# Kernel tuning notes

Measured on AMD Instinct MI355X. Metric: run time of the kernel, lower is better.

## Reference

```python
import jax, jax.numpy as jnp
import numpy as np

LOCAL_SIZE = 128
LN_EPS = 1e-5


def _ln(x):
    # F.layer_norm over last axis, no affine params
    mu = jnp.mean(x, axis=-1, keepdims=True)
    var = jnp.var(x, axis=-1, keepdims=True)
    return (x - mu) / jnp.sqrt(var + LN_EPS)


def _rel_shift(x):
    # x: [b, n, qlen, klen] -> Transformer-XL relative shift
    b, n, q, k = x.shape
    xp = jnp.pad(x, ((0, 0), (0, 0), (0, 0), (1, 0)))
    xp = xp.reshape(b, n, k + 1, q)
    return xp[:, :, 1:, :].reshape(b, n, q, k)


def setup_inputs() -> dict:
    key = jax.random.key(0)
    ks = jax.random.split(key, 12)
    bsz, d_model, qlen, mlen = 16, 1024, 256, 256
    n_head, d_head, d_inner = 16, 64, 4096
    klen = qlen + mlen
    s = 0.02  # param init scale
    return {
        "z1ss": jax.random.normal(ks[0], (bsz, d_model, qlen), jnp.float32),
        "uss": jax.random.normal(ks[1], (bsz, 3 * n_head * d_head, klen), jnp.float32) * 0.1,
        "mems": jax.random.normal(ks[2], (bsz, d_model, mlen), jnp.float32),
        "pos_emb": jax.random.normal(ks[3], (d_model, klen), jnp.float32),
        "Wqkv": jax.random.normal(ks[4], (3 * n_head * d_head, d_model), jnp.float32) * s,
        "Wr": jax.random.normal(ks[5], (n_head * d_head, d_model), jnp.float32) * s,
        "Wo": jax.random.normal(ks[6], (d_model, n_head * d_head), jnp.float32) * s,
        "bo": jnp.zeros((d_model,), jnp.float32),
        "r_w_bias": jax.random.uniform(ks[7], (n_head, d_head), jnp.float32, -0.05, 0.05),
        "r_r_bias": jax.random.uniform(ks[8], (n_head, d_head), jnp.float32, -0.05, 0.05),
        "W1": jax.random.normal(ks[9], (d_inner, d_model), jnp.float32) * s,
        "b1": jnp.zeros((d_inner,), jnp.float32),
        "W2": jax.random.normal(ks[10], (d_model, d_inner), jnp.float32) * s,
        "b2": jnp.zeros((d_model,), jnp.float32),
    }


def reference(z1ss, uss, mems, pos_emb, Wqkv, Wr, Wo, bo, r_w_bias, r_r_bias, W1, b1, W2, b2):
    bsz, d_model, qlen = z1ss.shape
    mlen = mems.shape[-1]
    n_head, d_head = r_w_bias.shape
    scale = 1.0 / (d_head ** 0.5)

    # ---- self-attention with relative positions ----
    cat = jnp.concatenate([mems, z1ss], axis=-1)            # [b, d, klen]
    klen = cat.shape[-1]
    w_heads = jnp.einsum('od,bdk->bok', Wqkv, cat) + uss     # [b, 3*n*dh, klen]
    r_head_k = (Wr @ pos_emb).reshape(n_head, d_head, -1)    # [n, dh, rlen]

    q, k, v = jnp.split(w_heads, 3, axis=1)
    q = q[:, :, -qlen:].reshape(bsz, n_head, d_head, qlen)   # [b, n, dh, q]
    k = k.reshape(bsz, n_head, d_head, klen)
    v = v.reshape(bsz, n_head, d_head, klen)

    AC = jnp.einsum('bndi,bndj->bnij', q + r_w_bias[:, :, None], k)
    BD = jnp.einsum('bndi,ndj->bnij', q + r_r_bias[:, :, None], r_head_k)
    BD = _rel_shift(BD)
    attn_score = (AC + BD) * scale                            # [b, n, q, klen]

    # causal + local-window mask
    i = jnp.arange(qlen)[:, None]
    j = jnp.arange(klen)[None, :]
    mask = (j > i + mlen) | (j <= i + mlen - LOCAL_SIZE)      # [q, klen]
    attn_score = jnp.where(mask[None, None], -1e30, attn_score)

    attn_prob = jax.nn.softmax(attn_score, axis=-1)
    attn_vec = jnp.einsum('bnij,bndj->bndi', attn_prob, v)    # [b, n, dh, q]
    attn_vec = attn_vec.reshape(bsz, n_head * d_head, qlen)
    attn_out = jnp.einsum('od,bdq->boq', Wo, attn_vec) + bo[None, :, None]

    # post-LN residual (pre_lnorm=False), work in [b, q, d]
    h = _ln((attn_out + z1ss).transpose(0, 2, 1))             # [b, q, d]

    # ---- position-wise FF ----
    ff = jax.nn.relu(jnp.einsum('bqd,id->bqi', h, W1) + b1)
    ff = jnp.einsum('bqi,di->bqd', ff, W2) + b2
    out = _ln(ff + h)                                          # [b, q, d]
    return out.transpose(0, 2, 1)                              # [b, d, q]
```

## Files before the change

### kernel.cpp

```cpp
#include <hip/hip_runtime.h>
#include <hip/hip_bf16.h>
#include <math.h>

#define BSZ    16
#define DMODEL 1024
#define QLEN   256
#define MLEN   256
#define KLEN   512
#define NHEAD  16
#define DHEAD  64
#define DINNER 4096

typedef __bf16 bf16;
typedef bf16 bf16x8 __attribute__((ext_vector_type(8)));
typedef float f32x4 __attribute__((ext_vector_type(4)));

#define GLOBAL_AS __attribute__((address_space(1)))
#define LDS_AS    __attribute__((address_space(3)))

__global__ __launch_bounds__(256) void prep_flat_k(
    const float* __restrict__ w0, const float* __restrict__ w1,
    const float* __restrict__ w2, const float* __restrict__ w3,
    const float* __restrict__ w4, const float* __restrict__ uss,
    bf16* __restrict__ o0, bf16* __restrict__ o1, bf16* __restrict__ o2,
    bf16* __restrict__ o3, bf16* __restrict__ o4, bf16* __restrict__ oV)
{
    long long i = (long long)blockIdx.x * 256 + threadIdx.x;
    const float* src; bf16* dst; long long soff, doff;
    if      (i <  786432) { src = w0; dst = o0; soff = doff = i; }
    else if (i < 1048576) { src = w1; dst = o1; soff = doff = i -  786432; }
    else if (i < 1310720) { src = w2; dst = o2; soff = doff = i - 1048576; }
    else if (i < 2359296) { src = w3; dst = o3; soff = doff = i - 1310720; }
    else if (i < 3407872) { src = w4; dst = o4; soff = doff = i - 2359296; }
    else {
        long long u = i - 3407872, b = u >> 17, r = u & 131071;
        src = uss; dst = oV; soff = b * 393216 + 262144 + r; doff = u;
    }
    float4 v = ((const float4*)src)[soff];
    bf16 b0 = (bf16)v.x, b1 = (bf16)v.y, b2 = (bf16)v.z, b3 = (bf16)v.w;
    union { ushort u[4]; uint2 d; } p;
    p.u[0] = *(ushort*)&b0; p.u[1] = *(ushort*)&b1;
    p.u[2] = *(ushort*)&b2; p.u[3] = *(ushort*)&b3;
    ((uint2*)dst)[doff] = p.d;
}

__global__ __launch_bounds__(256) void prep_tr_k(
    const float* __restrict__ mems, const float* __restrict__ z1ss,
    const float* __restrict__ pos_emb, const float* __restrict__ uss,
    bf16* __restrict__ catT, bf16* __restrict__ posT,
    bf16* __restrict__ ussQ, bf16* __restrict__ ussK)
{
    __shared__ float tile[32][33];
    int blk = blockIdx.x;
    const float* src; bf16* dst; long long soff, dof; int ld, ldo, tr, tc;
    if (blk < 8192) {
        int bh = blk >> 8, t = blk & 255;
        int b = bh >> 1, half = bh & 1;
        tr = t >> 3; tc = t & 7;
        src = half ? z1ss : mems; soff = (long long)b * 1024 * 256; ld = 256;
        dst = catT; dof = ((long long)b * 512 + half * 256) * 1024; ldo = 1024;
    } else if (blk < 8704) {
        int u = blk - 8192; tr = u >> 4; tc = u & 15;
        src = pos_emb; soff = 0; ld = 512;
        dst = posT; dof = 0; ldo = 1024;
    } else if (blk < 12800) {
        int u = blk - 8704; int b = u >> 8, t = u & 255;
        tr = t >> 3; tc = t & 7;
        src = uss; soff = (long long)b * 3072 * 512 + 256; ld = 512;
        dst = ussQ; dof = (long long)b * 256 * 1024; ldo = 1024;
    } else {
        int u = blk - 12800; int b = u >> 9, t = u & 511;
        tr = t >> 4; tc = t & 15;
        src = uss; soff = ((long long)b * 3072 + 1024) * 512; ld = 512;
        dst = ussK; dof = (long long)b * 512 * 1024; ldo = 1024;
    }
    int tx = threadIdx.x & 31, ty = threadIdx.x >> 5;
    const float* ip = src + soff;
#pragma unroll
    for (int yy = ty; yy < 32; yy += 8)
        tile[yy][tx] = ip[(long long)(tr * 32 + yy) * ld + tc * 32 + tx];
    __syncthreads();
#pragma unroll
    for (int yy = ty; yy < 32; yy += 8)
        dst[dof + (long long)(tc * 32 + yy) * ldo + tr * 32 + tx] = (bf16)tile[tx][yy];
}

__global__ __launch_bounds__(256) void gemm_bf16(
    const bf16* __restrict__ A, long long aBatch,
    const bf16* __restrict__ B, long long bBatch,
    int M, int N, int K, int kChunk,
    const float* __restrict__ bias,
    const bf16* __restrict__ Eb, long long ebBatch,
    int relu,
    float* __restrict__ outF, long long ofBatch,
    bf16* __restrict__ outB, long long obBatch,
    int omode, bf16* __restrict__ outB2,
    const bf16* __restrict__ EbQ, const bf16* __restrict__ EbK,
    const bf16* __restrict__ A2, const bf16* __restrict__ B2,
    bf16* __restrict__ O2)
{
    int t = threadIdx.x;
    int w = t >> 6, lane = t & 63;
    int m0 = blockIdx.y * 128, n0 = blockIdx.x * 128;
    int bz = blockIdx.z;
    bool rhk = (omode == 1) && (bz == 16);

    if (omode == 1 && !rhk && m0 < 256 && n0 < 1024) return;
    if (rhk && n0 >= 1024) return;

    __shared__ bf16 lA[128 * 32];
    __shared__ bf16 lB[128 * 32];

    const bf16* Ap; const bf16* Bp;
    float* oF = outF;
    bf16*  oB = outB;
    const bf16* Ebp = Eb;
    int Keff = K;
    if (rhk) {
        Ap = A2; Bp = B2;
    } else if (kChunk > 0) {
        Ap = A + (long long)bz * kChunk;
        Bp = B + (long long)bz * kChunk;
        if (outF) oF = outF + (long long)bz * ofBatch;
        Keff = kChunk;
    } else {
        Ap = A + (long long)bz * aBatch;
        Bp = B + (long long)bz * bBatch;
        if (Eb)   Ebp = Eb + (long long)bz * ebBatch;
        if (outF) oF = outF + (long long)bz * ofBatch;
        if (outB && omode == 0) oB = outB + (long long)bz * obBatch;
    }

    int q = lane >> 4, r16 = lane & 15;
    int wm = w >> 1, wn = w & 1;

    f32x4 acc[4][4];
#pragma unroll
    for (int i = 0; i < 4; ++i)
#pragma unroll
        for (int j = 0; j < 4; ++j)
            acc[i][j] = (f32x4){0.f, 0.f, 0.f, 0.f};

    int srow = (lane >> 2);
    int scol = (lane & 3) * 8;

    for (int k0 = 0; k0 < Keff; k0 += 32) {
        __syncthreads();
#pragma unroll
        for (int issue = 0; issue < 2; ++issue) {
            int c = issue * 4 + w;
            int row = c * 16 + srow;
            __builtin_amdgcn_global_load_lds(
                (const GLOBAL_AS void*)(Ap + (long long)(m0 + row) * K + k0 + scol),
                (LDS_AS void*)(lA + c * 512 + lane * 8), 16, 0, 0);
            __builtin_amdgcn_global_load_lds(
                (const GLOBAL_AS void*)(Bp + (long long)(n0 + row) * K + k0 + scol),
                (LDS_AS void*)(lB + c * 512 + lane * 8), 16, 0, 0);
        }
        __syncthreads();

        bf16x8 af[4], bfr[4];
#pragma unroll
        for (int i = 0; i < 4; ++i)
            af[i] = *(const bf16x8*)&lA[(wm * 64 + i * 16 + r16) * 32 + q * 8];
#pragma unroll
        for (int j = 0; j < 4; ++j)
            bfr[j] = *(const bf16x8*)&lB[(wn * 64 + j * 16 + r16) * 32 + q * 8];
#pragma unroll
        for (int i = 0; i < 4; ++i)
#pragma unroll
            for (int j = 0; j < 4; ++j)
                acc[i][j] = __builtin_amdgcn_mfma_f32_16x16x32_bf16(
                    af[i], bfr[j], acc[i][j], 0, 0, 0);
    }

#pragma unroll
    for (int i = 0; i < 4; ++i) {
#pragma unroll
        for (int r = 0; r < 4; ++r) {
            int m = m0 + wm * 64 + i * 16 + q * 4 + r;
#pragma unroll
            for (int j = 0; j < 4; ++j) {
                int n = n0 + wn * 64 + j * 16 + r16;
                float v = acc[i][j][r];
                if (bias) v += bias[n];
                if (relu) v = fmaxf(v, 0.f);
                if (rhk) {
                    O2[(long long)m * 1024 + n] = (bf16)v;
                } else if (omode == 1) {
                    if (n < 1024) {
                        if (m >= 256) {
                            long long idx = ((long long)(bz * 256 + m - 256) << 10) + n;
                            outB[idx] = (bf16)(v + (float)EbQ[idx]);
                        }
                    } else {
                        long long idx = ((long long)(bz * 512 + m) << 10) + (n - 1024);
                        outB2[idx] = (bf16)(v + (float)EbK[idx]);
                    }
                } else {
                    if (Eb) v += (float)Ebp[(long long)m * N + n];
                    if (oF) oF[(long long)m * N + n] = v;
                    if (oB) oB[(long long)m * N + n] = (bf16)v;
                }
            }
        }
    }
}

__global__ __launch_bounds__(256) void attn_mfma_k(
    const bf16* __restrict__ qT,
    const bf16* __restrict__ kT,
    const bf16* __restrict__ vB,
    const bf16* __restrict__ rhkT,
    const float* __restrict__ rwb,
    const float* __restrict__ rrb,
    bf16* __restrict__ avT)
{
    __shared__ float sBD[64][132];

    int t = threadIdx.x;
    int w = t >> 6, lane = t & 63;
    int lo = lane & 15, hi = lane >> 4;
    int i0 = blockIdx.x * 64;
    int n  = blockIdx.y;
    int b  = blockIdx.z;

    const bf16* qp = qT + ((long long)(b * 256 + i0 + 16 * w + lo)) * 1024 + n * 64;
    bf16x8 qw[2], qr[2];
#pragma unroll
    for (int ks = 0; ks < 2; ++ks) {
        bf16x8 qv = *(const bf16x8*)(qp + ks * 32 + hi * 8);
        const float* wb = rwb + n * 64 + ks * 32 + hi * 8;
        const float* rb = rrb + n * 64 + ks * 32 + hi * 8;
#pragma unroll
        for (int e = 0; e < 8; ++e) {
            float qf = (float)qv[e];
            qw[ks][e] = (bf16)(qf + wb[e]);
            qr[ks][e] = (bf16)(qf + rb[e]);
        }
    }

    const bf16* rp = rhkT + (long long)384 * 1024 + n * 64;
#pragma unroll
    for (int tj = 0; tj < 8; ++tj) {
        const bf16* bp = rp + (long long)(16 * tj + lo) * 1024;
        f32x4 a = (f32x4){0.f, 0.f, 0.f, 0.f};
        a = __builtin_amdgcn_mfma_f32_16x16x32_bf16(qr[0], *(const bf16x8*)(bp + hi * 8), a, 0, 0, 0);
        a = __builtin_amdgcn_mfma_f32_16x16x32_bf16(qr[1], *(const bf16x8*)(bp + 32 + hi * 8), a, 0, 0, 0);
#pragma unroll
        for (int r = 0; r < 4; ++r)
            sBD[16 * w + hi * 4 + r][16 * tj + lo] = a[r];
    }
    __syncthreads();

    f32x4 ac[12];
    const bf16* kp = kT + ((long long)b * 512 + i0 + 129) * 1024 + n * 64;
#pragma unroll
    for (int tj = 0; tj < 12; ++tj) {
        const bf16* bp = kp + (long long)(16 * tj + lo) * 1024;
        f32x4 a = (f32x4){0.f, 0.f, 0.f, 0.f};
        a = __builtin_amdgcn_mfma_f32_16x16x32_bf16(qw[0], *(const bf16x8*)(bp + hi * 8), a, 0, 0, 0);
        a = __builtin_amdgcn_mfma_f32_16x16x32_bf16(qw[1], *(const bf16x8*)(bp + 32 + hi * 8), a, 0, 0, 0);
        ac[tj] = a;
    }

    float p[12][4], rowmax[4], rowsum[4];
#pragma unroll
    for (int r = 0; r < 4; ++r) rowmax[r] = -1e30f;
#pragma unroll
    for (int tj = 0; tj < 12; ++tj) {
#pragma unroll
        for (int r = 0; r < 4; ++r) {
            int m = 16 * w + hi * 4 + r;
            int jj = 16 * tj + lo;
            int tt = jj - m;
            float v = (tt >= 0 && tt < 128) ? (ac[tj][r] + sBD[m][tt]) * 0.125f
                                            : -1e30f;
            p[tj][r] = v;
            rowmax[r] = fmaxf(rowmax[r], v);
        }
    }
#pragma unroll
    for (int r = 0; r < 4; ++r) {
        float mx = rowmax[r];
#pragma unroll
        for (int msk = 1; msk < 16; msk <<= 1)
            mx = fmaxf(mx, __shfl_xor(mx, msk, 64));
        rowmax[r] = mx;
        rowsum[r] = 0.f;
    }
#pragma unroll
    for (int tj = 0; tj < 12; ++tj) {
#pragma unroll
        for (int r = 0; r < 4; ++r) {
            float e = exp2f((p[tj][r] - rowmax[r]) * 1.44269504f);
            p[tj][r] = e;
            rowsum[r] += e;
        }
    }
#pragma unroll
    for (int r = 0; r < 4; ++r) {
        float s = rowsum[r];
#pragma unroll
        for (int msk = 1; msk < 16; msk <<= 1)
            s += __shfl_xor(s, msk, 64);
        rowsum[r] = 1.f / s;
    }

    bf16* P = (bf16*)&sBD[0][0];
#pragma unroll
    for (int tj = 0; tj < 12; ++tj) {
#pragma unroll
        for (int r = 0; r < 4; ++r) {
            int m = 16 * w + hi * 4 + r;
            P[m * 264 + 16 * tj + lo] = (bf16)(p[tj][r] * rowsum[r]);
        }
    }
    __syncthreads();

    f32x4 oacc[4];
#pragma unroll
    for (int td = 0; td < 4; ++td) oacc[td] = (f32x4){0.f, 0.f, 0.f, 0.f};
    const bf16* vp = vB + ((long long)b * 1024 + n * 64) * 512 + i0 + 129;
#pragma unroll
    for (int ks = 0; ks < 6; ++ks) {
        bf16x8 af = *(const bf16x8*)(P + (16 * w + lo) * 264 + ks * 32 + hi * 8);
#pragma unroll
        for (int td = 0; td < 4; ++td) {
            bf16x8 bv = *(const bf16x8*)(vp + (long long)(16 * td + lo) * 512 + ks * 32 + hi * 8);
            oacc[td] = __builtin_amdgcn_mfma_f32_16x16x32_bf16(af, bv, oacc[td], 0, 0, 0);
        }
    }
    bf16* op = avT + ((long long)(b * 256 + i0 + 16 * w)) * 1024 + n * 64;
#pragma unroll
    for (int td = 0; td < 4; ++td)
#pragma unroll
        for (int r = 0; r < 4; ++r)
            op[(long long)(hi * 4 + r) * 1024 + 16 * td + lo] = (bf16)oacc[td][r];
}

__global__ __launch_bounds__(256) void ln_bf16_k(
    const float* __restrict__ X1a, const float* __restrict__ X1b,
    const float* __restrict__ bo,  const bf16* __restrict__ catT,
    bf16* __restrict__ H)
{
    int row = blockIdx.x, t = threadIdx.x;
    __shared__ float r1[256], r2[256];
    const float* xa = X1a + (long long)row * 1024;
    const float* xb = X1b + (long long)row * 1024;
    const bf16*  zr = catT + ((long long)(row >> 8) * 512 + 256 + (row & 255)) * 1024;
    float v[4], s = 0.f, ss = 0.f;
#pragma unroll
    for (int u = 0; u < 4; ++u) {
        int c = t + u * 256;
        v[u] = xa[c] + xb[c] + bo[c] + (float)zr[c];
        s += v[u]; ss += v[u] * v[u];
    }
    r1[t] = s; r2[t] = ss;
    __syncthreads();
    for (int off = 128; off > 0; off >>= 1) {
        if (t < off) { r1[t] += r1[t + off]; r2[t] += r2[t + off]; }
        __syncthreads();
    }
    float mean = r1[0] * (1.f / 1024.f);
    float var  = r2[0] * (1.f / 1024.f) - mean * mean;
    float rstd = rsqrtf(var + 1e-5f);
    bf16* hr = H + (long long)row * 1024;
#pragma unroll
    for (int u = 0; u < 4; ++u)
        hr[t + u * 256] = (bf16)((v[u] - mean) * rstd);
}

__global__ __launch_bounds__(256) void ln_final_k(
    const bf16* __restrict__ Hb,
    const float* __restrict__ X2a, const float* __restrict__ X2b,
    const float* __restrict__ b2,
    float* __restrict__ O)
{
    int row = blockIdx.x, t = threadIdx.x;
    int b = row >> 8, qq = row & 255;
    __shared__ float r1[256], r2[256];
    const float* xa = X2a + (long long)row * 1024;
    const float* xb = X2b + (long long)row * 1024;
    const bf16*  hr = Hb  + (long long)row * 1024;

    float y[4], s = 0.f, ss = 0.f;
#pragma unroll
    for (int u = 0; u < 4; ++u) {
        int c = t + u * 256;
        y[u] = xa[c] + xb[c] + b2[c] + (float)hr[c];
        s += y[u]; ss += y[u] * y[u];
    }
    r1[t] = s; r2[t] = ss;
    __syncthreads();
    for (int off = 128; off > 0; off >>= 1) {
        if (t < off) { r1[t] += r1[t + off]; r2[t] += r2[t + off]; }
        __syncthreads();
    }
    float mean = r1[0] * (1.f / 1024.f);
    float var  = r2[0] * (1.f / 1024.f) - mean * mean;
    float rstd = rsqrtf(var + 1e-5f);

    float* ob = O + (long long)b * 1024 * 256 + qq;
#pragma unroll
    for (int u = 0; u < 4; ++u)
        ob[(long long)(t + u * 256) * 256] = (y[u] - mean) * rstd;
}

extern "C" void kernel_launch(void* const* d_in, const int* in_sizes, int n_in,
                              void* d_out, int out_size, void* d_ws, size_t ws_size,
                              hipStream_t stream) {
    const float* z1ss    = (const float*)d_in[0];
    const float* uss     = (const float*)d_in[1];
    const float* mems    = (const float*)d_in[2];
    const float* pos_emb = (const float*)d_in[3];
    const float* Wqkv    = (const float*)d_in[4];
    const float* Wr      = (const float*)d_in[5];
    const float* Wo      = (const float*)d_in[6];
    const float* bo      = (const float*)d_in[7];
    const float* rwb     = (const float*)d_in[8];
    const float* rrb     = (const float*)d_in[9];
    const float* W1      = (const float*)d_in[10];
    const float* b1      = (const float*)d_in[11];
    const float* W2      = (const float*)d_in[12];
    const float* b2      = (const float*)d_in[13];

    char* base = (char*)d_ws;
    bf16*  catT  = (bf16*) (base + 0);
    bf16*  posT  = (bf16*) (base + 16777216);
    bf16*  WqkvB = (bf16*) (base + 17825792);
    bf16*  WrB   = (bf16*) (base + 24117248);
    bf16*  WoB   = (bf16*) (base + 26214400);
    bf16*  W1B   = (bf16*) (base + 28311552);
    bf16*  W2B   = (bf16*) (base + 36700160);
    bf16*  qTB   = (bf16*) (base + 45088768);
    bf16*  kTB   = (bf16*) (base + 53477376);
    bf16*  vBB   = (bf16*) (base + 70254592);
    float* x1a   = (float*)(base + 53477376);
    float* x1b   = (float*)(base + 70254592);
    bf16*  ff_b  = (bf16*) (base + 53477376);
    bf16*  rhkTB = (bf16*) (base + 87031808);
    bf16*  avTB  = (bf16*) (base + 88080384);
    bf16*  ussQb = (bf16*) (base + 96468992);
    bf16*  ussKb = (bf16*) (base + 104857600);
    bf16*  ussVb = (bf16*) (base + 121634816);
    float* x2a   = (float*)(base + 96468992);
    float* x2b   = (float*)(base + 113246208);
    bf16*  hB    = (bf16*) (base + 130023424);

    prep_flat_k<<<21504, 256, 0, stream>>>(
        Wqkv, Wr, Wo, W1, W2, uss, WqkvB, WrB, WoB, W1B, W2B, ussVb);

    prep_tr_k<<<20992, 256, 0, stream>>>(
        mems, z1ss, pos_emb, uss, catT, posT, ussQb, ussKb);

    gemm_bf16<<<dim3(16, 4, 17), 256, 0, stream>>>(
        catT, 512LL * 1024, WqkvB, 0,
        512, 2048, 1024, 0,
        nullptr, nullptr, 0, 0,
        nullptr, 0, qTB, 0,
        1, kTB, ussQb, ussKb, posT, WrB, rhkTB);

    gemm_bf16<<<dim3(4, 8, BSZ), 256, 0, stream>>>(
        WqkvB + 2048 * 1024, 0, catT, 512LL * 1024,
        1024, 512, 1024, 0,
        nullptr, ussVb, 1024LL * 512, 0,
        nullptr, 0, vBB, 1024LL * 512,
        0, nullptr, nullptr, nullptr, nullptr, nullptr, nullptr);

    attn_mfma_k<<<dim3(4, NHEAD, BSZ), 256, 0, stream>>>(
        qTB, kTB, vBB, rhkTB, rwb, rrb, avTB);

    gemm_bf16<<<dim3(8, 32, 2), 256, 0, stream>>>(
        avTB, 0, WoB, 0,
        4096, 1024, 1024, 512,
        nullptr, nullptr, 0, 0,
        x1a, (long long)(x1b - x1a), nullptr, 0,
        0, nullptr, nullptr, nullptr, nullptr, nullptr, nullptr);

    ln_bf16_k<<<4096, 256, 0, stream>>>(x1a, x1b, bo, catT, hB);

    gemm_bf16<<<dim3(32, 32, 1), 256, 0, stream>>>(
        hB, 0, W1B, 0,
        4096, 4096, 1024, 0,
        b1, nullptr, 0, 1,
        nullptr, 0, ff_b, 0,
        0, nullptr, nullptr, nullptr, nullptr, nullptr, nullptr);

    gemm_bf16<<<dim3(8, 32, 2), 256, 0, stream>>>(
        ff_b, 0, W2B, 0,
        4096, 1024, 4096, 2048,
        nullptr, nullptr, 0, 0,
        x2a, (long long)(x2b - x2a), nullptr, 0,
        0, nullptr, nullptr, nullptr, nullptr, nullptr, nullptr);

    ln_final_k<<<4096, 256, 0, stream>>>(hB, x2a, x2b, b2, (float*)d_out);
}
```

Measured before the change: 682.7 us.

## Merge prep kernels, fuse QKV/V/Rhead GEMMs into one launch, widen K-step to 64

Combines the two input-preparation kernels into one launch and merges the QKV, positional-key and value projections into a single kernel with a compact block index map, so no launched blocks exit immediately. All GEMMs now stage a 64-wide K slice per barrier pair instead of 32, halving the number of syncs per tile at the cost of doubled LDS use per block. Fewer launches reduce launch gaps and tail effects, while the larger LDS footprint may reduce occupancy.

```diff
diff --git a/kernel.cpp b/kernel.cpp
--- a/kernel.cpp
+++ b/kernel.cpp
@@ -18,40 +18,39 @@
 #define GLOBAL_AS __attribute__((address_space(1)))
 #define LDS_AS    __attribute__((address_space(3)))
 
-__global__ __launch_bounds__(256) void prep_flat_k(
-    const float* __restrict__ w0, const float* __restrict__ w1,
-    const float* __restrict__ w2, const float* __restrict__ w3,
-    const float* __restrict__ w4, const float* __restrict__ uss,
-    bf16* __restrict__ o0, bf16* __restrict__ o1, bf16* __restrict__ o2,
-    bf16* __restrict__ o3, bf16* __restrict__ o4, bf16* __restrict__ oV)
+__global__ __launch_bounds__(256) void prep_k(
+    const float* __restrict__ Wqkv, const float* __restrict__ Wr,
+    const float* __restrict__ Wo,   const float* __restrict__ W1,
+    const float* __restrict__ W2,   const float* __restrict__ uss,
+    const float* __restrict__ mems, const float* __restrict__ z1ss,
+    const float* __restrict__ pos_emb,
+    bf16* __restrict__ WqkvB, bf16* __restrict__ WrB, bf16* __restrict__ WoB,
+    bf16* __restrict__ W1B,   bf16* __restrict__ W2B, bf16* __restrict__ ussV,
+    bf16* __restrict__ catT,  bf16* __restrict__ posT,
+    bf16* __restrict__ ussQ,  bf16* __restrict__ ussK)
 {
-    long long i = (long long)blockIdx.x * 256 + threadIdx.x;
-    const float* src; bf16* dst; long long soff, doff;
-    if      (i <  786432) { src = w0; dst = o0; soff = doff = i; }
-    else if (i < 1048576) { src = w1; dst = o1; soff = doff = i -  786432; }
-    else if (i < 1310720) { src = w2; dst = o2; soff = doff = i - 1048576; }
-    else if (i < 2359296) { src = w3; dst = o3; soff = doff = i - 1310720; }
-    else if (i < 3407872) { src = w4; dst = o4; soff = doff = i - 2359296; }
-    else {
-        long long u = i - 3407872, b = u >> 17, r = u & 131071;
-        src = uss; dst = oV; soff = b * 393216 + 262144 + r; doff = u;
-    }
-    float4 v = ((const float4*)src)[soff];
-    bf16 b0 = (bf16)v.x, b1 = (bf16)v.y, b2 = (bf16)v.z, b3 = (bf16)v.w;
-    union { ushort u[4]; uint2 d; } p;
-    p.u[0] = *(ushort*)&b0; p.u[1] = *(ushort*)&b1;
-    p.u[2] = *(ushort*)&b2; p.u[3] = *(ushort*)&b3;
-    ((uint2*)dst)[doff] = p.d;
-}
-
-__global__ __launch_bounds__(256) void prep_tr_k(
-    const float* __restrict__ mems, const float* __restrict__ z1ss,
-    const float* __restrict__ pos_emb, const float* __restrict__ uss,
-    bf16* __restrict__ catT, bf16* __restrict__ posT,
-    bf16* __restrict__ ussQ, bf16* __restrict__ ussK)
-{
+    if (blockIdx.x < 21504) {
+        long long i = (long long)blockIdx.x * 256 + threadIdx.x;
+        const float* src; bf16* dst; long long soff, doff;
+        if      (i <  786432) { src = Wqkv; dst = WqkvB; soff = doff = i; }
+        else if (i < 1048576) { src = Wr;   dst = WrB;   soff = doff = i -  786432; }
+        else if (i < 1310720) { src = Wo;   dst = WoB;   soff = doff = i - 1048576; }
+        else if (i < 2359296) { src = W1;   dst = W1B;   soff = doff = i - 1310720; }
+        else if (i < 3407872) { src = W2;   dst = W2B;   soff = doff = i - 2359296; }
+        else {
+            long long u = i - 3407872, b = u >> 17, r = u & 131071;
+            src = uss; dst = ussV; soff = b * 393216 + 262144 + r; doff = u;
+        }
+        float4 v = ((const float4*)src)[soff];
+        bf16 b0 = (bf16)v.x, b1 = (bf16)v.y, b2 = (bf16)v.z, b3 = (bf16)v.w;
+        union { ushort u[4]; uint2 d; } p;
+        p.u[0] = *(ushort*)&b0; p.u[1] = *(ushort*)&b1;
+        p.u[2] = *(ushort*)&b2; p.u[3] = *(ushort*)&b3;
+        ((uint2*)dst)[doff] = p.d;
+        return;
+    }
     __shared__ float tile[32][33];
-    int blk = blockIdx.x;
+    int blk = blockIdx.x - 21504;
     const float* src; bf16* dst; long long soff, dof; int ld, ldo, tr, tc;
     if (blk < 8192) {
         int bh = blk >> 8, t = blk & 255;
@@ -85,50 +84,137 @@
         dst[dof + (long long)(tc * 32 + yy) * ldo + tr * 32 + tx] = (bf16)tile[tx][yy];
 }
 
+__global__ __launch_bounds__(256) void qkv_gemm_k(
+    const bf16* __restrict__ catT, const bf16* __restrict__ WqkvB,
+    const bf16* __restrict__ posT, const bf16* __restrict__ WrB,
+    const bf16* __restrict__ ussQ, const bf16* __restrict__ ussK,
+    const bf16* __restrict__ ussV,
+    bf16* __restrict__ qT, bf16* __restrict__ kT,
+    bf16* __restrict__ rhkT, bf16* __restrict__ vB)
+{
+    __shared__ bf16 lA[2 * 128 * 32];
+    __shared__ bf16 lB[2 * 128 * 32];
+
+    int id = blockIdx.x;
+    int t = threadIdx.x;
+    int w = t >> 6, lane = t & 63;
+
+    const bf16 *Ap, *Bp;
+    int mode, bz = 0, m0, n0;
+    if (id < 768) {
+        bz = id / 48; int r = id % 48;
+        if (r < 32) { m0 = 256 + ((r >> 4) << 7); n0 = (r & 15) << 7; }
+        else        { int rr = r - 32; m0 = (rr >> 3) << 7; n0 = (8 + (rr & 7)) << 7; }
+        Ap = catT + (long long)bz * 512 * 1024; Bp = WqkvB; mode = 0;
+    } else if (id < 800) {
+        int rr = id - 768; m0 = (rr >> 3) << 7; n0 = (rr & 7) << 7;
+        Ap = posT; Bp = WrB; mode = 1;
+    } else {
+        int rr = id - 800; bz = rr >> 5; int tt = rr & 31;
+        m0 = (tt >> 2) << 7; n0 = (tt & 3) << 7;
+        Ap = WqkvB + 2048 * 1024; Bp = catT + (long long)bz * 512 * 1024; mode = 2;
+    }
+
+    int q = lane >> 4, r16 = lane & 15;
+    int wm = w >> 1, wn = w & 1;
+
+    f32x4 acc[4][4];
+#pragma unroll
+    for (int i = 0; i < 4; ++i)
+#pragma unroll
+        for (int j = 0; j < 4; ++j)
+            acc[i][j] = (f32x4){0.f, 0.f, 0.f, 0.f};
+
+    int srow = lane >> 2;
+    int scol = (lane & 3) * 8;
+
+    for (int k0 = 0; k0 < 1024; k0 += 64) {
+        __syncthreads();
+#pragma unroll
+        for (int half = 0; half < 2; ++half) {
+#pragma unroll
+            for (int issue = 0; issue < 2; ++issue) {
+                int c = issue * 4 + w;
+                int row = c * 16 + srow;
+                int col = k0 + half * 32 + scol;
+                __builtin_amdgcn_global_load_lds(
+                    (const GLOBAL_AS void*)(Ap + (long long)(m0 + row) * 1024 + col),
+                    (LDS_AS void*)(lA + half * 4096 + c * 512 + lane * 8), 16, 0, 0);
+                __builtin_amdgcn_global_load_lds(
+                    (const GLOBAL_AS void*)(Bp + (long long)(n0 + row) * 1024 + col),
+                    (LDS_AS void*)(lB + half * 4096 + c * 512 + lane * 8), 16, 0, 0);
+            }
+        }
+        __syncthreads();
+#pragma unroll
+        for (int kh = 0; kh < 2; ++kh) {
+            bf16x8 af[4], bfr[4];
+#pragma unroll
+            for (int i = 0; i < 4; ++i)
+                af[i] = *(const bf16x8*)&lA[kh * 4096 + (wm * 64 + i * 16 + r16) * 32 + q * 8];
+#pragma unroll
+            for (int j = 0; j < 4; ++j)
+                bfr[j] = *(const bf16x8*)&lB[kh * 4096 + (wn * 64 + j * 16 + r16) * 32 + q * 8];
+#pragma unroll
+            for (int i = 0; i < 4; ++i)
+#pragma unroll
+                for (int j = 0; j < 4; ++j)
+                    acc[i][j] = __builtin_amdgcn_mfma_f32_16x16x32_bf16(
+                        af[i], bfr[j], acc[i][j], 0, 0, 0);
+        }
+    }
+
+    bool isq = (mode == 0) && (n0 < 1024);
+#pragma unroll
+    for (int i = 0; i < 4; ++i) {
+#pragma unroll
+        for (int r = 0; r < 4; ++r) {
+            int m = m0 + wm * 64 + i * 16 + q * 4 + r;
+#pragma unroll
+            for (int j = 0; j < 4; ++j) {
+                int n = n0 + wn * 64 + j * 16 + r16;
+                float v = acc[i][j][r];
+                if (mode == 1) {
+                    rhkT[(long long)m * 1024 + n] = (bf16)v;
+                } else if (mode == 2) {
+                    long long idx = ((long long)bz * 1024 + m) * 512 + n;
+                    vB[idx] = (bf16)(v + (float)ussV[idx]);
+                } else if (isq) {
+                    long long idx = ((long long)(bz * 256 + m - 256) << 10) + n;
+                    qT[idx] = (bf16)(v + (float)ussQ[idx]);
+                } else {
+                    long long idx = ((long long)(bz * 512 + m) << 10) + (n - 1024);
+                    kT[idx] = (bf16)(v + (float)ussK[idx]);
+                }
+            }
+        }
+    }
+}
+
 __global__ __launch_bounds__(256) void gemm_bf16(
-    const bf16* __restrict__ A, long long aBatch,
-    const bf16* __restrict__ B, long long bBatch,
+    const bf16* __restrict__ A, const bf16* __restrict__ B,
     int M, int N, int K, int kChunk,
-    const float* __restrict__ bias,
-    const bf16* __restrict__ Eb, long long ebBatch,
-    int relu,
+    const float* __restrict__ bias, int relu,
     float* __restrict__ outF, long long ofBatch,
-    bf16* __restrict__ outB, long long obBatch,
-    int omode, bf16* __restrict__ outB2,
-    const bf16* __restrict__ EbQ, const bf16* __restrict__ EbK,
-    const bf16* __restrict__ A2, const bf16* __restrict__ B2,
-    bf16* __restrict__ O2)
+    bf16* __restrict__ outB)
 {
+    __shared__ bf16 lA[2 * 128 * 32];
+    __shared__ bf16 lB[2 * 128 * 32];
+
     int t = threadIdx.x;
     int w = t >> 6, lane = t & 63;
     int m0 = blockIdx.y * 128, n0 = blockIdx.x * 128;
     int bz = blockIdx.z;
-    bool rhk = (omode == 1) && (bz == 16);
-
-    if (omode == 1 && !rhk && m0 < 256 && n0 < 1024) return;
-    if (rhk && n0 >= 1024) return;
-
-    __shared__ bf16 lA[128 * 32];
-    __shared__ bf16 lB[128 * 32];
-
-    const bf16* Ap; const bf16* Bp;
+
+    const bf16* Ap = A;
+    const bf16* Bp = B;
     float* oF = outF;
-    bf16*  oB = outB;
-    const bf16* Ebp = Eb;
     int Keff = K;
-    if (rhk) {
-        Ap = A2; Bp = B2;
-    } else if (kChunk > 0) {
+    if (kChunk > 0) {
         Ap = A + (long long)bz * kChunk;
         Bp = B + (long long)bz * kChunk;
         if (outF) oF = outF + (long long)bz * ofBatch;
         Keff = kChunk;
-    } else {
-        Ap = A + (long long)bz * aBatch;
-        Bp = B + (long long)bz * bBatch;
-        if (Eb)   Ebp = Eb + (long long)bz * ebBatch;
-        if (outF) oF = outF + (long long)bz * ofBatch;
-        if (outB && omode == 0) oB = outB + (long long)bz * obBatch;
     }
 
     int q = lane >> 4, r16 = lane & 15;
@@ -141,37 +227,43 @@
         for (int j = 0; j < 4; ++j)
             acc[i][j] = (f32x4){0.f, 0.f, 0.f, 0.f};
 
-    int srow = (lane >> 2);
+    int srow = lane >> 2;
     int scol = (lane & 3) * 8;
 
-    for (int k0 = 0; k0 < Keff; k0 += 32) {
+    for (int k0 = 0; k0 < Keff; k0 += 64) {
         __syncthreads();
 #pragma unroll
-        for (int issue = 0; issue < 2; ++issue) {
-            int c = issue * 4 + w;
-            int row = c * 16 + srow;
-            __builtin_amdgcn_global_load_lds(
-                (const GLOBAL_AS void*)(Ap + (long long)(m0 + row) * K + k0 + scol),
-                (LDS_AS void*)(lA + c * 512 + lane * 8), 16, 0, 0);
-            __builtin_amdgcn_global_load_lds(
-                (const GLOBAL_AS void*)(Bp + (long long)(n0 + row) * K + k0 + scol),
-                (LDS_AS void*)(lB + c * 512 + lane * 8), 16, 0, 0);
+        for (int half = 0; half < 2; ++half) {
+#pragma unroll
+            for (int issue = 0; issue < 2; ++issue) {
+                int c = issue * 4 + w;
+                int row = c * 16 + srow;
+                int col = k0 + half * 32 + scol;
+                __builtin_amdgcn_global_load_lds(
+                    (const GLOBAL_AS void*)(Ap + (long long)(m0 + row) * K + col),
+                    (LDS_AS void*)(lA + half * 4096 + c * 512 + lane * 8), 16, 0, 0);
+                __builtin_amdgcn_global_load_lds(
+                    (const GLOBAL_AS void*)(Bp + (long long)(n0 + row) * K + col),
+                    (LDS_AS void*)(lB + half * 4096 + c * 512 + lane * 8), 16, 0, 0);
+            }
         }
         __syncthreads();
-
-        bf16x8 af[4], bfr[4];
-#pragma unroll
-        for (int i = 0; i < 4; ++i)
-            af[i] = *(const bf16x8*)&lA[(wm * 64 + i * 16 + r16) * 32 + q * 8];
-#pragma unroll
-        for (int j = 0; j < 4; ++j)
-            bfr[j] = *(const bf16x8*)&lB[(wn * 64 + j * 16 + r16) * 32 + q * 8];
-#pragma unroll
-        for (int i = 0; i < 4; ++i)
+#pragma unroll
+        for (int kh = 0; kh < 2; ++kh) {
+            bf16x8 af[4], bfr[4];
+#pragma unroll
+            for (int i = 0; i < 4; ++i)
+                af[i] = *(const bf16x8*)&lA[kh * 4096 + (wm * 64 + i * 16 + r16) * 32 + q * 8];
 #pragma unroll
             for (int j = 0; j < 4; ++j)
-                acc[i][j] = __builtin_amdgcn_mfma_f32_16x16x32_bf16(
-                    af[i], bfr[j], acc[i][j], 0, 0, 0);
+                bfr[j] = *(const bf16x8*)&lB[kh * 4096 + (wn * 64 + j * 16 + r16) * 32 + q * 8];
+#pragma unroll
+            for (int i = 0; i < 4; ++i)
+#pragma unroll
+                for (int j = 0; j < 4; ++j)
+                    acc[i][j] = __builtin_amdgcn_mfma_f32_16x16x32_bf16(
+                        af[i], bfr[j], acc[i][j], 0, 0, 0);
+        }
     }
 
 #pragma unroll
@@ -185,23 +277,8 @@
                 float v = acc[i][j][r];
                 if (bias) v += bias[n];
                 if (relu) v = fmaxf(v, 0.f);
-                if (rhk) {
-                    O2[(long long)m * 1024 + n] = (bf16)v;
-                } else if (omode == 1) {
-                    if (n < 1024) {
-                        if (m >= 256) {
-                            long long idx = ((long long)(bz * 256 + m - 256) << 10) + n;
-                            outB[idx] = (bf16)(v + (float)EbQ[idx]);
-                        }
-                    } else {
-                        long long idx = ((long long)(bz * 512 + m) << 10) + (n - 1024);
-                        outB2[idx] = (bf16)(v + (float)EbK[idx]);
-                    }
-                } else {
-                    if (Eb) v += (float)Ebp[(long long)m * N + n];
-                    if (oF) oF[(long long)m * N + n] = v;
-                    if (oB) oB[(long long)m * N + n] = (bf16)v;
-                }
+                if (oF)   oF[(long long)m * N + n] = v;
+                if (outB) outB[(long long)m * N + n] = (bf16)v;
             }
         }
     }
@@ -448,51 +525,29 @@
     float* x2b   = (float*)(base + 113246208);
     bf16*  hB    = (bf16*) (base + 130023424);
 
-    prep_flat_k<<<21504, 256, 0, stream>>>(
-        Wqkv, Wr, Wo, W1, W2, uss, WqkvB, WrB, WoB, W1B, W2B, ussVb);
-
-    prep_tr_k<<<20992, 256, 0, stream>>>(
-        mems, z1ss, pos_emb, uss, catT, posT, ussQb, ussKb);
-
-    gemm_bf16<<<dim3(16, 4, 17), 256, 0, stream>>>(
-        catT, 512LL * 1024, WqkvB, 0,
-        512, 2048, 1024, 0,
-        nullptr, nullptr, 0, 0,
-        nullptr, 0, qTB, 0,
-        1, kTB, ussQb, ussKb, posT, WrB, rhkTB);
-
-    gemm_bf16<<<dim3(4, 8, BSZ), 256, 0, stream>>>(
-        WqkvB + 2048 * 1024, 0, catT, 512LL * 1024,
-        1024, 512, 1024, 0,
-        nullptr, ussVb, 1024LL * 512, 0,
-        nullptr, 0, vBB, 1024LL * 512,
-        0, nullptr, nullptr, nullptr, nullptr, nullptr, nullptr);
+    prep_k<<<42496, 256, 0, stream>>>(
+        Wqkv, Wr, Wo, W1, W2, uss, mems, z1ss, pos_emb,
+        WqkvB, WrB, WoB, W1B, W2B, ussVb, catT, posT, ussQb, ussKb);
+
+    qkv_gemm_k<<<1312, 256, 0, stream>>>(
+        catT, WqkvB, posT, WrB, ussQb, ussKb, ussVb, qTB, kTB, rhkTB, vBB);
 
     attn_mfma_k<<<dim3(4, NHEAD, BSZ), 256, 0, stream>>>(
         qTB, kTB, vBB, rhkTB, rwb, rrb, avTB);
 
     gemm_bf16<<<dim3(8, 32, 2), 256, 0, stream>>>(
-        avTB, 0, WoB, 0,
-        4096, 1024, 1024, 512,
-        nullptr, nullptr, 0, 0,
-        x1a, (long long)(x1b - x1a), nullptr, 0,
-        0, nullptr, nullptr, nullptr, nullptr, nullptr, nullptr);
+        avTB, WoB, 4096, 1024, 1024, 512,
+        nullptr, 0, x1a, (long long)(x1b - x1a), nullptr);
 
     ln_bf16_k<<<4096, 256, 0, stream>>>(x1a, x1b, bo, catT, hB);
 
     gemm_bf16<<<dim3(32, 32, 1), 256, 0, stream>>>(
-        hB, 0, W1B, 0,
-        4096, 4096, 1024, 0,
-        b1, nullptr, 0, 1,
-        nullptr, 0, ff_b, 0,
-        0, nullptr, nullptr, nullptr, nullptr, nullptr, nullptr);
+        hB, W1B, 4096, 4096, 1024, 0,
+        b1, 1, nullptr, 0, ff_b);
 
     gemm_bf16<<<dim3(8, 32, 2), 256, 0, stream>>>(
-        ff_b, 0, W2B, 0,
-        4096, 1024, 4096, 2048,
-        nullptr, nullptr, 0, 0,
-        x2a, (long long)(x2b - x2a), nullptr, 0,
-        0, nullptr, nullptr, nullptr, nullptr, nullptr, nullptr);
+        ff_b, W2B, 4096, 1024, 4096, 2048,
+        nullptr, 0, x2a, (long long)(x2b - x2a), nullptr);
 
     ln_final_k<<<4096, 256, 0, stream>>>(hB, x2a, x2b, b2, (float*)d_out);
 }
```

Result: faster. 600.1 us (-12.1%).
